# Performance work log

Hardware: AMD Instinct MI355X
Metric: run time of the kernel (lower is better)

Reference implementation:

```python
import jax, jax.numpy as jnp
import numpy as np

F_IN, H, D, C, NCLS = 1024, 512, 256, 10, 4


def setup_inputs() -> dict:
    key = jax.random.key(0)
    ks = jax.random.split(key, 20)
    N = 32768
    x_path = jax.random.normal(ks[0], (N, F_IN), dtype=jnp.float32)
    cluster_id = jax.random.randint(ks[1], (N,), 0, C, dtype=jnp.int64)
    s1 = 1.0 / np.sqrt(F_IN)
    s2 = 1.0 / np.sqrt(H)
    s3 = 1.0 / np.sqrt(D)
    return {
        "x_path": x_path,
        "cluster_id": cluster_id,
        "W1": jax.random.normal(ks[2], (C, F_IN, H), dtype=jnp.float32) * s1,
        "b1": jnp.zeros((C, H), dtype=jnp.float32),
        "W2": jax.random.normal(ks[3], (C, H, H), dtype=jnp.float32) * s2,
        "b2": jnp.zeros((C, H), dtype=jnp.float32),
        "fc_W": jax.random.normal(ks[4], (H, H), dtype=jnp.float32) * s2,
        "fc_b": jnp.zeros((H,), dtype=jnp.float32),
        "a_W": jax.random.normal(ks[5], (H, D), dtype=jnp.float32) * s2,
        "a_b": jnp.zeros((D,), dtype=jnp.float32),
        "g_W": jax.random.normal(ks[6], (H, D), dtype=jnp.float32) * s2,
        "g_b": jnp.zeros((D,), dtype=jnp.float32),
        "c_W": jax.random.normal(ks[7], (D, 1), dtype=jnp.float32) * s3,
        "c_b": jnp.zeros((1,), dtype=jnp.float32),
        "rho_W": jax.random.normal(ks[8], (H, D), dtype=jnp.float32) * s2,
        "rho_b": jnp.zeros((D,), dtype=jnp.float32),
        "cls_W": jax.random.normal(ks[9], (D, NCLS), dtype=jnp.float32) * s3,
        "cls_b": jnp.zeros((NCLS,), dtype=jnp.float32),
    }


def reference(x_path, cluster_id, W1, b1, W2, b2, fc_W, fc_b, a_W, a_b,
              g_W, g_b, c_W, c_b, rho_W, rho_b, cls_W, cls_b):
    relu = jax.nn.relu
    means = []
    for i in range(C):  # fixed small set of clusters (structurally distinct MLPs)
        m = (cluster_id == i).astype(x_path.dtype)          # [N]
        y = relu(relu(x_path @ W1[i] + b1[i]) @ W2[i] + b2[i])  # [N, H]
        cnt = jnp.maximum(m.sum(), 1.0)
        means.append((y * m[:, None]).sum(axis=0) / cnt)    # [H] segment mean
    h_cluster = jnp.stack(means, axis=0)                    # [C, H]
    h = relu(h_cluster @ fc_W + fc_b)                       # [C, H]
    a = jnp.tanh(h @ a_W + a_b)                             # [C, D]
    g = jax.nn.sigmoid(h @ g_W + g_b)                       # [C, D]
    A = (a * g) @ c_W + c_b                                 # [C, 1]
    A = jax.nn.softmax(A.T, axis=1)                         # [1, C]
    h_path = A @ h                                          # [1, H]
    h_path = relu(h_path @ rho_W + rho_b).squeeze()         # [D]
    logits = (h_path @ cls_W + cls_b)[None, :]              # [1, NCLS]
    Y_hat = jnp.argmax(logits, axis=1, keepdims=True)       # [1, 1]
    hazards = jax.nn.sigmoid(logits)
    S = jnp.cumprod(1.0 - hazards, axis=1)
    return hazards, S, Y_hat
```

## Files before the change

### kernel.cpp

```cpp
#include <hip/hip_runtime.h>
#include <hip/hip_fp16.h>
#include <math.h>

#define FIN 1024
#define H 512
#define DD 256
#define NCLS 4
#define MAXC 64

#define TMM 32
#define WCOLS 40

#define WS_TOFF 1088
#define WS_NZ   1408
#define WS_SUMS 1536

typedef _Float16 f16x8 __attribute__((ext_vector_type(8)));
typedef _Float16 f16x4 __attribute__((ext_vector_type(4)));
typedef _Float16 f16x2 __attribute__((ext_vector_type(2)));
typedef float    f32x4 __attribute__((ext_vector_type(4)));

__global__ void detect_kernel(const int* __restrict__ cid32, int* flag, int n) {
    int i = blockIdx.x * blockDim.x + threadIdx.x;
    bool p = (i < n) && (i & 1) && (cid32[i] != 0);
    unsigned long long m = __ballot(p);
    if (p && ((threadIdx.x & 63) == (__ffsll(m) - 1))) atomicOr(flag, 1);
}

__device__ __forceinline__ int get_cid(const int* cid, int flag, int i) {
    return flag ? cid[i] : cid[2 * i];
}

__global__ void count_kernel(const int* __restrict__ cid, const int* __restrict__ flag,
                             int* counts, int n, int C) {
    __shared__ int lc[MAXC];
    int tid = threadIdx.x;
    if (tid < C) lc[tid] = 0;
    __syncthreads();
    int i = blockIdx.x * blockDim.x + tid;
    if (i < n) {
        int c = get_cid(cid, *flag, i);
        if ((unsigned)c < (unsigned)C) atomicAdd(&lc[c], 1);
    }
    __syncthreads();
    if (tid < C && lc[tid] > 0) atomicAdd(&counts[tid], lc[tid]);
}

__global__ void offsets_kernel(const int* __restrict__ counts, int* offs, int* toff,
                               int C, int tilesz) {
    if (threadIdx.x == 0 && blockIdx.x == 0) {
        int s = 0, ts = 0;
        offs[0] = 0; toff[0] = 0;
        for (int c = 0; c < C; c++) {
            s += counts[c];                          offs[c + 1] = s;
            ts += (counts[c] + tilesz - 1) / tilesz; toff[c + 1] = ts;
        }
    }
}

__global__ void compact_kernel(const int* __restrict__ cid, const int* __restrict__ flag,
                               const int* __restrict__ offs, int* cursor,
                               int* lists, int n, int C) {
    __shared__ int lc[MAXC], lbase[MAXC], lpos[MAXC];
    int tid = threadIdx.x;
    if (tid < C) { lc[tid] = 0; lpos[tid] = 0; }
    __syncthreads();
    int i = blockIdx.x * blockDim.x + tid;
    int c = -1;
    if (i < n) {
        int cc = get_cid(cid, *flag, i);
        if ((unsigned)cc < (unsigned)C) { c = cc; atomicAdd(&lc[c], 1); }
    }
    __syncthreads();
    if (tid < C && lc[tid] > 0) lbase[tid] = atomicAdd(&cursor[tid], lc[tid]);
    __syncthreads();
    if (c >= 0) {
        int p = atomicAdd(&lpos[c], 1);
        lists[offs[c] + lbase[c] + p] = i;
    }
}


__device__ __forceinline__ int frag_off(int r, int g) {
    int blk = r >> 1;
    int slot = (((r & 1) << 2) | g) ^ (blk & 7);
    return blk * 128 + slot * 16;
}

__device__ __forceinline__ void gload1k(const char* g, char* l) {
    __builtin_amdgcn_global_load_lds(
        (const __attribute__((address_space(1))) void*)g,
        (__attribute__((address_space(3))) void*)l, 16, 0, 0);
}

__device__ __forceinline__ void wprep_body(
    const float* __restrict__ W, _Float16* __restrict__ hi,
    _Float16* __restrict__ lo, int K, int b, float sw[32][132], int tid)
{
    int ktn = K >> 5;
    int c = b / (4 * ktn);
    int rem = b % (4 * ktn);
    int nb = rem / ktn, kt = rem % ktn;
    const float* Wc = W + (size_t)c * K * H + (size_t)(kt * 32) * H + nb * 128;
#pragma unroll
    for (int it = 0; it < 4; it++) {
        int id = it * 256 + tid;
        int r = id >> 5, c4 = (id & 31) * 4;
        *(float4*)&sw[r][c4] = *(const float4*)(Wc + (size_t)r * H + c4);
    }
    __syncthreads();
    size_t tile = ((size_t)(c * 4 + nb)) * ktn + kt;
    char* hp = (char*)hi + tile * 8192;
    char* lp = (char*)lo + tile * 8192;
#pragma unroll
    for (int it = 0; it < 2; it++) {
        int fi = it * 256 + tid;
        int cl = fi >> 2, g = fi & 3;
        f16x8 hv, lv;
#pragma unroll
        for (int e = 0; e < 8; e++) {
            float v = sw[g * 8 + e][cl];
            _Float16 h = (_Float16)v;
            hv[e] = h;
            lv[e] = (_Float16)(v - (float)h);
        }
        int off = frag_off(cl, g);
        *(f16x8*)(hp + off) = hv;
        *(f16x8*)(lp + off) = lv;
    }
}

__global__ __launch_bounds__(256) void wprep_both(
    const float* __restrict__ W1, _Float16* __restrict__ w1h, _Float16* __restrict__ w1l,
    const float* __restrict__ W2, _Float16* __restrict__ w2h, _Float16* __restrict__ w2l,
    int C)
{
    __shared__ float sw[32][132];
    int n1 = C * 4 * (FIN / 32);
    int b = blockIdx.x;
    int tid = threadIdx.x;
    if (b < n1) wprep_body(W1, w1h, w1l, FIN, b, sw, tid);
    else        wprep_body(W2, w2h, w2l, H, b - n1, sw, tid);
}

struct __align__(16) GSmem {
    union {
        struct { _Float16 A[2][4096]; _Float16 Bh[2][4096]; _Float16 Bl[2][4096]; } s;
        _Float16 Ct[128][132];
    } u;
    int sIdx[128];
};

__global__ __launch_bounds__(256, 3) void gemm1(
    const float* __restrict__ x,
    const int* __restrict__ counts, const int* __restrict__ offs,
    const int* __restrict__ toff, const int* __restrict__ lists,
    const _Float16* __restrict__ wh, const _Float16* __restrict__ wl,
    const float* __restrict__ b1, _Float16* __restrict__ h1,
    int C, int nwg)
{
    int bid = blockIdx.x;
    {
        int q = nwg >> 3, r = nwg & 7, xcd = bid & 7, k = bid >> 3;
        bid = (xcd < r ? xcd * (q + 1) : r * (q + 1) + (xcd - r) * q) + k;
    }
    int ntile = toff[C];
    if (bid >= ntile * 4) return;
    int t = bid >> 2, nb = bid & 3;
    int c = 0;
    while (c + 1 < C && t >= toff[c + 1]) c++;
    int cnt = counts[c];
    int row0 = (t - toff[c]) * 128;

    __shared__ GSmem sm;
    int tid = threadIdx.x;
    int lane = tid & 63;
    int wave = __builtin_amdgcn_readfirstlane(tid >> 6);
    if (tid < 128) {
        int r = row0 + tid;
        sm.sIdx[tid] = (r < cnt) ? lists[offs[c] + r] : -1;
    }
    __syncthreads();

    int r0 = tid >> 2, g0 = tid & 3;
    int gi0 = sm.sIdx[r0], gi1 = sm.sIdx[64 + r0];
    const float* xp0 = x + (size_t)(gi0 < 0 ? 0 : gi0) * FIN + g0 * 8;
    const float* xp1 = x + (size_t)(gi1 < 0 ? 0 : gi1) * FIN + g0 * 8;
    int aoff0 = frag_off(r0, g0), aoff1 = frag_off(64 + r0, g0);

    const char* gh = (const char*)wh + ((size_t)(c * 4 + nb) * 32) * 8192;
    const char* gl = (const char*)wl + ((size_t)(c * 4 + nb) * 32) * 8192;
    char* ldsA  = (char*)sm.u.s.A;
    char* ldsBh = (char*)sm.u.s.Bh;
    char* ldsBl = (char*)sm.u.s.Bl;
    int ch = wave * 2;

    int wr = wave >> 1, wq = wave & 1;
    int l15 = lane & 15, g = lane >> 4;

    f32x4 acc[4][4];
#pragma unroll
    for (int i = 0; i < 4; i++)
#pragma unroll
        for (int j = 0; j < 4; j++) acc[i][j] = (f32x4){0.f, 0.f, 0.f, 0.f};

    {
        const char* gsh = gh + ch * 1024 + lane * 16;
        const char* gsl = gl + ch * 1024 + lane * 16;
        gload1k(gsh,        ldsBh + ch * 1024);
        gload1k(gsh + 1024, ldsBh + ch * 1024 + 1024);
        gload1k(gsl,        ldsBl + ch * 1024);
        gload1k(gsl + 1024, ldsBl + ch * 1024 + 1024);
        float4 v0a = make_float4(0.f,0.f,0.f,0.f), v0b = v0a, v1a = v0a, v1b = v0a;
        if (gi0 >= 0) { v0a = *(const float4*)xp0; v0b = *(const float4*)(xp0 + 4); }
        if (gi1 >= 0) { v1a = *(const float4*)xp1; v1b = *(const float4*)(xp1 + 4); }
        f16x8 a0 = { (_Float16)v0a.x, (_Float16)v0a.y, (_Float16)v0a.z, (_Float16)v0a.w,
                     (_Float16)v0b.x, (_Float16)v0b.y, (_Float16)v0b.z, (_Float16)v0b.w };
        f16x8 a1 = { (_Float16)v1a.x, (_Float16)v1a.y, (_Float16)v1a.z, (_Float16)v1a.w,
                     (_Float16)v1b.x, (_Float16)v1b.y, (_Float16)v1b.z, (_Float16)v1b.w };
        *(f16x8*)(ldsA + aoff0) = a0;
        *(f16x8*)(ldsA + aoff1) = a1;
        xp0 += 32; xp1 += 32;
    }
    __syncthreads();

    int cur = 0;
    for (int kt = 0; kt < 32; kt++) {
        int nxt = cur ^ 1;
        bool pf = kt < 31;
        float4 v0a = make_float4(0.f,0.f,0.f,0.f), v0b = v0a, v1a = v0a, v1b = v0a;
        if (pf) {
            const char* gsh = gh + (size_t)(kt + 1) * 8192 + ch * 1024 + lane * 16;
            const char* gsl = gl + (size_t)(kt + 1) * 8192 + ch * 1024 + lane * 16;
            gload1k(gsh,        ldsBh + nxt * 8192 + ch * 1024);
            gload1k(gsh + 1024, ldsBh + nxt * 8192 + ch * 1024 + 1024);
            gload1k(gsl,        ldsBl + nxt * 8192 + ch * 1024);
            gload1k(gsl + 1024, ldsBl + nxt * 8192 + ch * 1024 + 1024);
            if (gi0 >= 0) { v0a = *(const float4*)xp0; v0b = *(const float4*)(xp0 + 4); }
            if (gi1 >= 0) { v1a = *(const float4*)xp1; v1b = *(const float4*)(xp1 + 4); }
            xp0 += 32; xp1 += 32;
        }
        f16x8 a[4], bh[4], bl[4];
#pragma unroll
        for (int fr = 0; fr < 4; fr++)
            a[fr] = *(const f16x8*)(ldsA + cur * 8192 + frag_off(wr * 64 + fr * 16 + l15, g));
#pragma unroll
        for (int fc = 0; fc < 4; fc++) {
            int col = wq * 64 + fc * 16 + l15;
            bh[fc] = *(const f16x8*)(ldsBh + cur * 8192 + frag_off(col, g));
            bl[fc] = *(const f16x8*)(ldsBl + cur * 8192 + frag_off(col, g));
        }
#pragma unroll
        for (int fr = 0; fr < 4; fr++)
#pragma unroll
            for (int fc = 0; fc < 4; fc++) {
                acc[fr][fc] = __builtin_amdgcn_mfma_f32_16x16x32_f16(a[fr], bh[fc], acc[fr][fc], 0, 0, 0);
                acc[fr][fc] = __builtin_amdgcn_mfma_f32_16x16x32_f16(a[fr], bl[fc], acc[fr][fc], 0, 0, 0);
            }
        if (pf) {
            f16x8 a0 = { (_Float16)v0a.x, (_Float16)v0a.y, (_Float16)v0a.z, (_Float16)v0a.w,
                         (_Float16)v0b.x, (_Float16)v0b.y, (_Float16)v0b.z, (_Float16)v0b.w };
            f16x8 a1 = { (_Float16)v1a.x, (_Float16)v1a.y, (_Float16)v1a.z, (_Float16)v1a.w,
                         (_Float16)v1b.x, (_Float16)v1b.y, (_Float16)v1b.z, (_Float16)v1b.w };
            *(f16x8*)(ldsA + nxt * 8192 + aoff0) = a0;
            *(f16x8*)(ldsA + nxt * 8192 + aoff1) = a1;
        }
        __syncthreads();
        cur = nxt;
    }
    __syncthreads();
    const float* b1c = b1 + (size_t)c * H + nb * 128;
#pragma unroll
    for (int fc = 0; fc < 4; fc++) {
        int colL = wq * 64 + fc * 16 + l15;
        float bv = b1c[colL];
#pragma unroll
        for (int fr = 0; fr < 4; fr++)
#pragma unroll
            for (int j = 0; j < 4; j++) {
                int rowL = wr * 64 + fr * 16 + g * 4 + j;
                float v = acc[fr][fc][j] + bv;
                sm.u.Ct[rowL][colL] = (_Float16)(v > 0.f ? v : 0.f);
            }
    }
    __syncthreads();
    char* hout = (char*)h1 + ((size_t)t * 16 + nb * 4) * 8192;
#pragma unroll
    for (int ktl = 0; ktl < 4; ktl++)
#pragma unroll
        for (int it = 0; it < 2; it++) {
            int fi = it * 256 + tid;
            int rl = fi >> 2, gg = fi & 3;
            f16x8 v = *(const f16x8*)&sm.u.Ct[rl][ktl * 32 + gg * 8];
            *(f16x8*)(hout + (size_t)ktl * 8192 + frag_off(rl, gg)) = v;
        }
}

__global__ __launch_bounds__(256, 3) void gemm2(
    const _Float16* __restrict__ h1,
    const int* __restrict__ counts, const int* __restrict__ toff,
    const _Float16* __restrict__ wh, const _Float16* __restrict__ wl,
    const float* __restrict__ b2, double* __restrict__ sums,
    int C, int nwg)
{
    int bid = blockIdx.x;
    {
        int q = nwg >> 3, r = nwg & 7, xcd = bid & 7, k = bid >> 3;
        bid = (xcd < r ? xcd * (q + 1) : r * (q + 1) + (xcd - r) * q) + k;
    }
    int ntile = toff[C];
    if (bid >= ntile * 4) return;
    int t = bid >> 2, nb = bid & 3;
    int c = 0;
    while (c + 1 < C && t >= toff[c + 1]) c++;
    int cnt = counts[c];
    int row0 = (t - toff[c]) * 128;

    __shared__ alignas(16) _Float16 sA2[2][4096];
    __shared__ alignas(16) _Float16 sBh2[2][4096];
    __shared__ alignas(16) _Float16 sBl2[2][4096];

    int tid = threadIdx.x;
    int lane = tid & 63;
    int wave = __builtin_amdgcn_readfirstlane(tid >> 6);
    int wr = wave >> 1, wq = wave & 1;
    int l15 = lane & 15, g = lane >> 4;
    int ch = wave * 2;

    const char* gA = (const char*)h1 + (size_t)t * 16 * 8192;
    const char* gh = (const char*)wh + ((size_t)(c * 4 + nb) * 16) * 8192;
    const char* gl = (const char*)wl + ((size_t)(c * 4 + nb) * 16) * 8192;

    f32x4 acc[4][4];
#pragma unroll
    for (int i = 0; i < 4; i++)
#pragma unroll
        for (int j = 0; j < 4; j++) acc[i][j] = (f32x4){0.f, 0.f, 0.f, 0.f};

    {
        const char* ga  = gA + ch * 1024 + lane * 16;
        const char* gsh = gh + ch * 1024 + lane * 16;
        const char* gsl = gl + ch * 1024 + lane * 16;
        gload1k(ga,         (char*)sA2  + ch * 1024);
        gload1k(ga + 1024,  (char*)sA2  + ch * 1024 + 1024);
        gload1k(gsh,        (char*)sBh2 + ch * 1024);
        gload1k(gsh + 1024, (char*)sBh2 + ch * 1024 + 1024);
        gload1k(gsl,        (char*)sBl2 + ch * 1024);
        gload1k(gsl + 1024, (char*)sBl2 + ch * 1024 + 1024);
    }
    __syncthreads();

    int cur = 0;
    for (int kt = 0; kt < 16; kt++) {
        int nxt = cur ^ 1;
        if (kt < 15) {
            const char* ga  = gA + (size_t)(kt + 1) * 8192 + ch * 1024 + lane * 16;
            const char* gsh = gh + (size_t)(kt + 1) * 8192 + ch * 1024 + lane * 16;
            const char* gsl = gl + (size_t)(kt + 1) * 8192 + ch * 1024 + lane * 16;
            gload1k(ga,         (char*)sA2  + nxt * 8192 + ch * 1024);
            gload1k(ga + 1024,  (char*)sA2  + nxt * 8192 + ch * 1024 + 1024);
            gload1k(gsh,        (char*)sBh2 + nxt * 8192 + ch * 1024);
            gload1k(gsh + 1024, (char*)sBh2 + nxt * 8192 + ch * 1024 + 1024);
            gload1k(gsl,        (char*)sBl2 + nxt * 8192 + ch * 1024);
            gload1k(gsl + 1024, (char*)sBl2 + nxt * 8192 + ch * 1024 + 1024);
        }
        f16x8 a[4], bh[4], bl[4];
#pragma unroll
        for (int fr = 0; fr < 4; fr++)
            a[fr] = *(const f16x8*)((char*)sA2 + cur * 8192 + frag_off(wr * 64 + fr * 16 + l15, g));
#pragma unroll
        for (int fc = 0; fc < 4; fc++) {
            int col = wq * 64 + fc * 16 + l15;
            bh[fc] = *(const f16x8*)((char*)sBh2 + cur * 8192 + frag_off(col, g));
            bl[fc] = *(const f16x8*)((char*)sBl2 + cur * 8192 + frag_off(col, g));
        }
#pragma unroll
        for (int fr = 0; fr < 4; fr++)
#pragma unroll
            for (int fc = 0; fc < 4; fc++) {
                acc[fr][fc] = __builtin_amdgcn_mfma_f32_16x16x32_f16(a[fr], bh[fc], acc[fr][fc], 0, 0, 0);
                acc[fr][fc] = __builtin_amdgcn_mfma_f32_16x16x32_f16(a[fr], bl[fc], acc[fr][fc], 0, 0, 0);
            }
        __syncthreads();
        cur = nxt;
    }
    const float* b2c = b2 + (size_t)c * H + nb * 128;
    int rbound = cnt - row0;
    float psum[4];
#pragma unroll
    for (int fc = 0; fc < 4; fc++) {
        int colL = wq * 64 + fc * 16 + l15;
        float bv = b2c[colL];
        float s = 0.f;
#pragma unroll
        for (int fr = 0; fr < 4; fr++)
#pragma unroll
            for (int j = 0; j < 4; j++) {
                int rowL = wr * 64 + fr * 16 + g * 4 + j;
                float v = acc[fr][fc][j] + bv;
                v = v > 0.f ? v : 0.f;
                if (rowL < rbound) s += v;
            }
        psum[fc] = s;
    }
#pragma unroll
    for (int fc = 0; fc < 4; fc++) {
        psum[fc] += __shfl_xor(psum[fc], 16);
        psum[fc] += __shfl_xor(psum[fc], 32);
    }
    if (g == 0) {
#pragma unroll
        for (int fc = 0; fc < 4; fc++)
            atomicAdd(&sums[(size_t)c * H + nb * 128 + wq * 64 + fc * 16 + l15],
                      (double)psum[fc]);
    }
}

__global__ __launch_bounds__(256) void wsplit_kernel(
    const float* __restrict__ W, _Float16* __restrict__ hi,
    _Float16* __restrict__ lo, int K, int N)
{
    __shared__ float tile[64][65];
    int tid = threadIdx.x;
    int tilesN = N >> 6, tilesK = K >> 6;
    int b = blockIdx.x;
    int c = b / (tilesK * tilesN);
    int r = b % (tilesK * tilesN);
    int tk = r / tilesN, tn = r % tilesN;
    const float* Wc = W + (size_t)c * K * N;
    int k0 = tk << 6, n0 = tn << 6;
#pragma unroll
    for (int it = 0; it < 16; it++) {
        int id = it * 256 + tid;
        int kr = id >> 6, nc = id & 63;
        tile[kr][nc] = Wc[(size_t)(k0 + kr) * N + n0 + nc];
    }
    __syncthreads();
    _Float16* hic = hi + (size_t)c * N * K;
    _Float16* loc = lo + (size_t)c * N * K;
#pragma unroll
    for (int it = 0; it < 8; it++) {
        int id = it * 256 + tid;
        int nc = id >> 5, kp = (id & 31) * 2;
        float a0 = tile[kp][nc], a1 = tile[kp + 1][nc];
        _Float16 h0 = (_Float16)a0, h1v = (_Float16)a1;
        _Float16 l0 = (_Float16)(a0 - (float)h0);
        _Float16 l1 = (_Float16)(a1 - (float)h1v);
        size_t off = (size_t)(n0 + nc) * K + k0 + kp;
        f16x2 hv = {h0, h1v}, lv = {l0, l1};
        *(f16x2*)(hic + off) = hv;
        *(f16x2*)(loc + off) = lv;
    }
}

struct __align__(16) MfmaSmem {
    _Float16 sW[2][128][WCOLS];
    _Float16 sH[TMM][520];
    _Float16 sX[TMM][WCOLS];
    int      sIdx[TMM];
};

__global__ __launch_bounds__(256, 2) void mlp_mfma(
    const float* __restrict__ x,
    const int* __restrict__ counts, const int* __restrict__ offs,
    const int* __restrict__ toff, const int* __restrict__ lists,
    const _Float16* __restrict__ w1h, const _Float16* __restrict__ w1l,
    const _Float16* __restrict__ w2h, const _Float16* __restrict__ w2l,
    const float* __restrict__ b1, const float* __restrict__ b2,
    double* __restrict__ sums, int C, int nwg)
{
    int bid = blockIdx.x;
    {
        int q = nwg >> 3, r = nwg & 7, xcd = bid & 7, k = bid >> 3;
        bid = (xcd < r ? xcd * (q + 1) : r * (q + 1) + (xcd - r) * q) + k;
    }
    if (bid >= toff[C]) return;
    int c = 0;
    while (c + 1 < C && bid >= toff[c + 1]) c++;
    int t = bid - toff[c];
    int cnt = counts[c];
    int row0 = t * TMM;

    __shared__ MfmaSmem sm;
    int tid  = threadIdx.x;
    int lane = tid & 63, wave = tid >> 6;
    int wr = wave >> 1, wq = wave & 1;
    int l15 = lane & 15, g = lane >> 4;

    if (tid < TMM) {
        int r = row0 + tid;
        sm.sIdx[tid] = (r < cnt) ? lists[offs[c] + r] : -1;
    }

    const _Float16* w1hc = w1h + (size_t)c * FIN * H;
    const _Float16* w1lc = w1l + (size_t)c * FIN * H;
    const _Float16* w2hc = w2h + (size_t)c * H * H;
    const _Float16* w2lc = w2l + (size_t)c * H * H;
    const float* b1c = b1 + (size_t)c * H;
    const float* b2c = b2 + (size_t)c * H;

    int xr = tid >> 3;
    int xk = (tid & 7) * 4;
    int s_lc = tid >> 2;
    int s_kc = (tid & 3) * 8;

    for (int nb = 0; nb < H; nb += 128) {
        f32x4 acc[4];
#pragma unroll
        for (int f = 0; f < 4; f++) acc[f] = (f32x4){0.f, 0.f, 0.f, 0.f};

        for (int kk = 0; kk < FIN; kk += 32) {
            __syncthreads();
            {
                int gi = sm.sIdx[xr];
                float4 v = make_float4(0.f, 0.f, 0.f, 0.f);
                if (gi >= 0) v = *(const float4*)(x + (size_t)gi * FIN + kk + xk);
                f16x4 hv = { (_Float16)v.x, (_Float16)v.y, (_Float16)v.z, (_Float16)v.w };
                *(f16x4*)&sm.sX[xr][xk] = hv;
            }
            {
                const _Float16* ph = w1hc + (size_t)(nb + s_lc) * FIN + kk + s_kc;
                const _Float16* pl = w1lc + (size_t)(nb + s_lc) * FIN + kk + s_kc;
                *(f16x8*)&sm.sW[0][s_lc][s_kc]      = *(const f16x8*)ph;
                *(f16x8*)&sm.sW[0][64 + s_lc][s_kc] = *(const f16x8*)(ph + (size_t)64 * FIN);
                *(f16x8*)&sm.sW[1][s_lc][s_kc]      = *(const f16x8*)pl;
                *(f16x8*)&sm.sW[1][64 + s_lc][s_kc] = *(const f16x8*)(pl + (size_t)64 * FIN);
            }
            __syncthreads();
            f16x8 a = *(const f16x8*)&sm.sX[wr * 16 + l15][g * 8];
#pragma unroll
            for (int f = 0; f < 4; f++) {
                int lc = wq * 64 + f * 16 + l15;
                f16x8 bh = *(const f16x8*)&sm.sW[0][lc][g * 8];
                f16x8 bl = *(const f16x8*)&sm.sW[1][lc][g * 8];
                acc[f] = __builtin_amdgcn_mfma_f32_16x16x32_f16(a, bh, acc[f], 0, 0, 0);
                acc[f] = __builtin_amdgcn_mfma_f32_16x16x32_f16(a, bl, acc[f], 0, 0, 0);
            }
        }
#pragma unroll
        for (int f = 0; f < 4; f++) {
            int col = nb + wq * 64 + f * 16 + l15;
            float bv = b1c[col];
#pragma unroll
            for (int j = 0; j < 4; j++) {
                int row = wr * 16 + g * 4 + j;
                float v = acc[f][j] + bv;
                sm.sH[row][col] = (_Float16)(v > 0.f ? v : 0.f);
            }
        }
    }

    for (int nb = 0; nb < H; nb += 128) {
        f32x4 acc[4];
#pragma unroll
        for (int f = 0; f < 4; f++) acc[f] = (f32x4){0.f, 0.f, 0.f, 0.f};

        for (int kk = 0; kk < H; kk += 32) {
            __syncthreads();
            {
                const _Float16* ph = w2hc + (size_t)(nb + s_lc) * H + kk + s_kc;
                const _Float16* pl = w2lc + (size_t)(nb + s_lc) * H + kk + s_kc;
                *(f16x8*)&sm.sW[0][s_lc][s_kc]      = *(const f16x8*)ph;
                *(f16x8*)&sm.sW[0][64 + s_lc][s_kc] = *(const f16x8*)(ph + (size_t)64 * H);
                *(f16x8*)&sm.sW[1][s_lc][s_kc]      = *(const f16x8*)pl;
                *(f16x8*)&sm.sW[1][64 + s_lc][s_kc] = *(const f16x8*)(pl + (size_t)64 * H);
            }
            __syncthreads();
            f16x8 a = *(const f16x8*)&sm.sH[wr * 16 + l15][kk + g * 8];
#pragma unroll
            for (int f = 0; f < 4; f++) {
                int lc = wq * 64 + f * 16 + l15;
                f16x8 bh = *(const f16x8*)&sm.sW[0][lc][g * 8];
                f16x8 bl = *(const f16x8*)&sm.sW[1][lc][g * 8];
                acc[f] = __builtin_amdgcn_mfma_f32_16x16x32_f16(a, bh, acc[f], 0, 0, 0);
                acc[f] = __builtin_amdgcn_mfma_f32_16x16x32_f16(a, bl, acc[f], 0, 0, 0);
            }
        }
        float psum[4];
#pragma unroll
        for (int f = 0; f < 4; f++) {
            int col = nb + wq * 64 + f * 16 + l15;
            float bv = b2c[col];
            float s = 0.f;
#pragma unroll
            for (int j = 0; j < 4; j++) {
                int row = wr * 16 + g * 4 + j;
                float v = acc[f][j] + bv;
                v = v > 0.f ? v : 0.f;
                if (sm.sIdx[row] >= 0) s += v;
            }
            psum[f] = s;
        }
#pragma unroll
        for (int f = 0; f < 4; f++) {
            psum[f] += __shfl_xor(psum[f], 16);
            psum[f] += __shfl_xor(psum[f], 32);
        }
        if (g == 0) {
#pragma unroll
            for (int f = 0; f < 4; f++) {
                int col = nb + wq * 64 + f * 16 + l15;
                atomicAdd(&sums[(size_t)c * H + col], (double)psum[f]);
            }
        }
    }
}

__global__ __launch_bounds__(256) void row_mlp(
    const float* __restrict__ x, const int* __restrict__ cid,
    const int* __restrict__ flag,
    const float* __restrict__ W1, const float* __restrict__ b1,
    const float* __restrict__ W2, const float* __restrict__ b2,
    double* __restrict__ sums, int n, int C)
{
    int r = blockIdx.x;
    if (r >= n) return;
    int c = get_cid(cid, *flag, r);
    if ((unsigned)c >= (unsigned)C) return;

    __shared__ float sx[FIN];
    __shared__ float sh[H];
    int tid = threadIdx.x;

    for (int i = tid; i < FIN; i += 256) sx[i] = x[(size_t)r * FIN + i];
    __syncthreads();

    const float* W1c = W1 + (size_t)c * FIN * H;
    const float* b1c = b1 + (size_t)c * H;
    for (int col = tid; col < H; col += 256) {
        float acc = 0.f;
        for (int k = 0; k < FIN; k++) acc += sx[k] * W1c[(size_t)k * H + col];
        acc += b1c[col];
        sh[col] = acc > 0.f ? acc : 0.f;
    }
    __syncthreads();

    const float* W2c = W2 + (size_t)c * H * H;
    const float* b2c = b2 + (size_t)c * H;
    for (int col = tid; col < H; col += 256) {
        float acc = 0.f;
        for (int k = 0; k < H; k++) acc += sh[k] * W2c[(size_t)k * H + col];
        acc += b2c[col];
        float y = acc > 0.f ? acc : 0.f;
        atomicAdd(&sums[(size_t)c * H + col], (double)y);
    }
}

__global__ __launch_bounds__(128) void tailA_kernel(
    const int* __restrict__ counts, const double* __restrict__ sums,
    const float* __restrict__ fcW, const float* __restrict__ fcb,
    double* __restrict__ h_ws, int* __restrict__ nzflag)
{
    int b = blockIdx.x;
    int c = b >> 2, ch = b & 3;
    int tid = threadIdx.x;
    __shared__ double shc[H];
    double denom = fmax((double)counts[c], 1.0);
    double nz = 0.0;
    for (int i = tid; i < H; i += 128) {
        double v = sums[(size_t)c * H + i];
        nz += fabs(v);
        shc[i] = v / denom;
    }
    if (ch == 0) {
        if (__any(nz != 0.0) && (tid & 63) == 0) atomicOr(nzflag, 1);
    }
    __syncthreads();
    int col = ch * 128 + tid;
    double acc = 0.0;
#pragma unroll 16
    for (int k = 0; k < H; k++) acc += shc[k] * (double)fcW[k * H + col];
    acc += (double)fcb[col];
    h_ws[(size_t)c * H + col] = acc > 0.0 ? acc : 0.0;
}

__global__ __launch_bounds__(128) void tailB_kernel(
    const double* __restrict__ h_ws,
    const float* __restrict__ aW, const float* __restrict__ ab,
    const float* __restrict__ gW, const float* __restrict__ gb,
    double* __restrict__ ag_ws)
{
    int b = blockIdx.x;
    int c = b >> 1, dh = b & 1;
    int tid = threadIdx.x;
    __shared__ double sh[H];
    for (int i = tid; i < H; i += 128) sh[i] = h_ws[(size_t)c * H + i];
    __syncthreads();
    int d = dh * 128 + tid;
    double aa = (double)ab[d], gg = (double)gb[d];
#pragma unroll 8
    for (int k = 0; k < H; k++) {
        double hv = sh[k];
        aa += hv * (double)aW[k * DD + d];
        gg += hv * (double)gW[k * DD + d];
    }
    ag_ws[(size_t)c * DD + d] = tanh(aa) / (1.0 + exp(-gg));
}

__global__ __launch_bounds__(256) void tailC_kernel(
    const double* __restrict__ h_ws, const double* __restrict__ ag_ws,
    const float* __restrict__ cW, const float* __restrict__ cb,
    const float* __restrict__ rhoW, const float* __restrict__ rhob,
    const float* __restrict__ clsW, const float* __restrict__ clsb,
    const int* __restrict__ counts, const int* __restrict__ nzflag,
    const int* __restrict__ cid_raw, int n, int C,
    float* __restrict__ out)
{
    int tid = threadIdx.x;
    int lane = tid & 63, w = tid >> 6;
    __shared__ double sA[MAXC];
    __shared__ double shp[H];
    __shared__ double sr[DD];
    __shared__ double lgs[NCLS];

    for (int c = w; c < C; c += 4) {
        double acc = 0.0;
        for (int d = lane; d < DD; d += 64)
            acc += ag_ws[(size_t)c * DD + d] * (double)cW[d];
#pragma unroll
        for (int off = 32; off >= 1; off >>= 1) acc += __shfl_xor(acc, off);
        if (lane == 0) sA[c] = acc + (double)cb[0];
    }
    __syncthreads();
    if (tid == 0) {
        double m = sA[0];
        for (int c = 1; c < C; c++) m = fmax(m, sA[c]);
        double s = 0.0;
        for (int c = 0; c < C; c++) { sA[c] = exp(sA[c] - m); s += sA[c]; }
        for (int c = 0; c < C; c++) sA[c] /= s;
    }
    __syncthreads();
    for (int col = tid; col < H; col += 256) {
        double s = 0.0;
        for (int c = 0; c < C; c++) s += sA[c] * h_ws[(size_t)c * H + col];
        shp[col] = s;
    }
    __syncthreads();
    {
        int d = tid;
        double acc = 0.0;
#pragma unroll 16
        for (int k = 0; k < H; k++) acc += shp[k] * (double)rhoW[k * DD + d];
        acc += (double)rhob[d];
        sr[d] = acc > 0.0 ? acc : 0.0;
    }
    __syncthreads();
    for (int kk = w; kk < NCLS; kk += 4) {
        double acc = 0.0;
        for (int d = lane; d < DD; d += 64)
            acc += sr[d] * (double)clsW[d * NCLS + kk];
#pragma unroll
        for (int off = 32; off >= 1; off >>= 1) acc += __shfl_xor(acc, off);
        if (lane == 0) lgs[kk] = acc + (double)clsb[kk];
    }
    __syncthreads();
    if (tid == 0) {
        int am = 0;
        double best = lgs[0];
        double run = 1.0;
        for (int kk = 0; kk < NCLS; kk++) {
            if (lgs[kk] > best) { best = lgs[kk]; am = kk; }
            double hz = 1.0 / (1.0 + exp(-lgs[kk]));
            out[kk] = (float)hz;
            run *= (1.0 - hz);
            out[NCLS + kk] = (float)run;
        }
        long long cnt_total = 0;
        for (int c = 0; c < C; c++) cnt_total += counts[c];
        float yout;
        if (cnt_total == 0) {
            yout = 4.0e6f + (float)((cid_raw[0] & 0xFFF) + 4096 * (cid_raw[1] & 0xFFF));
        } else if (cnt_total != (long long)n) {
            yout = 2.0e6f + (float)cnt_total;
        } else if (*nzflag == 0) {
            yout = 3.0e6f;
        } else {
            yout = (float)am;
        }
        out[2 * NCLS] = yout;
    }
}

__global__ void diag_kernel(float* __restrict__ out, float code) {
    if (threadIdx.x == 0) {
        double run = 1.0;
        for (int kk = 0; kk < NCLS; kk++) {
            out[kk] = 0.5f;
            run *= 0.5;
            out[NCLS + kk] = (float)run;
        }
        out[2 * NCLS] = code;
    }
}

extern "C" void kernel_launch(void* const* d_in, const int* in_sizes, int n_in,
                              void* d_out, int out_size, void* d_ws, size_t ws_size,
                              hipStream_t stream) {
    const float* x    = (const float*)d_in[0];
    const int*   cid  = (const int*)d_in[1];
    const float* W1   = (const float*)d_in[2];
    const float* b1   = (const float*)d_in[3];
    const float* W2   = (const float*)d_in[4];
    const float* b2   = (const float*)d_in[5];
    const float* fcW  = (const float*)d_in[6];
    const float* fcb  = (const float*)d_in[7];
    const float* aW   = (const float*)d_in[8];
    const float* ab   = (const float*)d_in[9];
    const float* gW   = (const float*)d_in[10];
    const float* gb   = (const float*)d_in[11];
    const float* cW   = (const float*)d_in[12];
    const float* cb   = (const float*)d_in[13];
    const float* rhoW = (const float*)d_in[14];
    const float* rhob = (const float*)d_in[15];
    const float* clsW = (const float*)d_in[16];
    const float* clsb = (const float*)d_in[17];
    float* out = (float*)d_out;

    long long n = in_sizes[1];
    long long C = (in_sizes[7] > 0) ? (long long)in_sizes[3] / in_sizes[7] : 0;
    bool shapes_ok =
        n > 0 &&
        (long long)in_sizes[0] == n * FIN &&
        in_sizes[7] == H && in_sizes[9] == DD && in_sizes[17] == NCLS &&
        C >= 1 && C <= MAXC &&
        (long long)in_sizes[2] == C * FIN * H &&
        (long long)in_sizes[4] == C * H * H;

    size_t hws_off   = WS_SUMS + (size_t)C * H * 8;
    size_t agws_off  = hws_off + (size_t)C * H * 8;
    size_t lists_off = agws_off + (size_t)C * DD * 8;
    size_t wt_off    = (lists_off + (size_t)n * 4 + 255) & ~(size_t)255;
    size_t w1t_bytes = (size_t)C * H * FIN * 2;
    size_t w2t_bytes = (size_t)C * H * H * 2;
    size_t w1h_off   = wt_off;
    size_t w1l_off   = w1h_off + w1t_bytes;
    size_t w2h_off   = w1l_off + w1t_bytes;
    size_t w2l_off   = w2h_off + w2t_bytes;
    size_t h1_off    = (w2l_off + w2t_bytes + 255) & ~(size_t)255;
    int    nn = (int)n, CC = (int)C;
    int    ntile_ub  = (nn + 127) / 128 + CC;
    size_t h1_bytes  = (size_t)ntile_ub * 16 * 8192;
    size_t ws_full   = h1_off + h1_bytes;
    size_t ws_mid    = h1_off;
    size_t ws_row    = lists_off;

    if (!shapes_ok) {
        diag_kernel<<<1, 64, 0, stream>>>(out, 7.0e6f + (float)(C >= 0 ? C : 0));
        return;
    }
    if (ws_size < ws_row) {
        diag_kernel<<<1, 64, 0, stream>>>(
            out, 6.0e6f + (float)(ws_size > 0 ? (ws_size >> 10) : 0));
        return;
    }

    char* ws = (char*)d_ws;
    int*    counts = (int*)ws;
    int*    flag   = (int*)(ws + 256);
    int*    cursor = (int*)(ws + 512);
    int*    offs   = (int*)(ws + 768);
    int*    toff   = (int*)(ws + WS_TOFF);
    int*    nzflag = (int*)(ws + WS_NZ);
    double* sums   = (double*)(ws + WS_SUMS);
    double* h_ws   = (double*)(ws + hws_off);
    double* ag_ws  = (double*)(ws + agws_off);
    int*    lists  = (int*)(ws + lists_off);
    _Float16* w1h  = (_Float16*)(ws + w1h_off);
    _Float16* w1l  = (_Float16*)(ws + w1l_off);
    _Float16* w2h  = (_Float16*)(ws + w2h_off);
    _Float16* w2l  = (_Float16*)(ws + w2l_off);
    _Float16* h1   = (_Float16*)(ws + h1_off);

    int nb = (nn + 255) / 256;

    hipMemsetAsync(ws, 0, hws_off, stream);

    detect_kernel<<<nb, 256, 0, stream>>>(cid, flag, nn);
    count_kernel<<<nb, 256, 0, stream>>>(cid, flag, counts, nn, CC);

    if (ws_size >= ws_full) {
        offsets_kernel<<<1, 64, 0, stream>>>(counts, offs, toff, CC, 128);
        compact_kernel<<<nb, 256, 0, stream>>>(cid, flag, offs, cursor, lists, nn, CC);
        wprep_both<<<CC * 4 * (FIN / 32 + H / 32), 256, 0, stream>>>(
            W1, w1h, w1l, W2, w2h, w2l, CC);
        int grid = ntile_ub * 4;
        gemm1<<<grid, 256, 0, stream>>>(x, counts, offs, toff, lists,
                                        w1h, w1l, b1, h1, CC, grid);
        gemm2<<<grid, 256, 0, stream>>>(h1, counts, toff, w2h, w2l, b2,
                                        sums, CC, grid);
    } else if (ws_size >= ws_mid) {
        offsets_kernel<<<1, 64, 0, stream>>>(counts, offs, toff, CC, TMM);
        compact_kernel<<<nb, 256, 0, stream>>>(cid, flag, offs, cursor, lists, nn, CC);
        wsplit_kernel<<<CC * (FIN / 64) * (H / 64), 256, 0, stream>>>(W1, w1h, w1l, FIN, H);
        wsplit_kernel<<<CC * (H / 64) * (H / 64), 256, 0, stream>>>(W2, w2h, w2l, H, H);
        int nt = (nn + TMM - 1) / TMM + CC;
        mlp_mfma<<<nt, 256, 0, stream>>>(x, counts, offs, toff, lists,
                                         w1h, w1l, w2h, w2l, b1, b2,
                                         sums, CC, nt);
    } else {
        row_mlp<<<nn, 256, 0, stream>>>(x, cid, flag, W1, b1, W2, b2, sums, nn, CC);
    }

    tailA_kernel<<<CC * 4, 128, 0, stream>>>(counts, sums, fcW, fcb, h_ws, nzflag);
    tailB_kernel<<<CC * 2, 128, 0, stream>>>(h_ws, aW, ab, gW, gb, ag_ws);
    tailC_kernel<<<1, 256, 0, stream>>>(h_ws, ag_ws, cW, cb, rhoW, rhob,
                                        clsW, clsb, counts, nzflag, cid,
                                        nn, CC, out);
}
```

Baseline: 526.1 us.

## Pre-convert x to fp16 and stream gathered rows directly into LDS in gemm1

Adds a pass that converts the fp32 input x to fp16 in workspace, plus a new gemm1 that gathers the rows via global_load_lds into a swizzled LDS layout instead of loading fp32 through registers and converting. The new kernel uses a single LDS buffer so occupancy can rise to 4 blocks per SM, and it points padding rows at a zeroed row. It costs an extra full read of x and a write of a half-size copy, and it needs a larger workspace. Without that workspace it falls back to the old register-path kernel.

```diff
diff --git a/kernel.cpp b/kernel.cpp
--- a/kernel.cpp
+++ b/kernel.cpp
@@ -80,11 +80,32 @@
     }
 }
 
+__global__ __launch_bounds__(256) void xprep_kernel(
+    const float* __restrict__ x, _Float16* __restrict__ x16, long long total8)
+{
+    long long stride = (long long)gridDim.x * 256;
+    for (long long i = blockIdx.x * 256LL + threadIdx.x; i < total8; i += stride) {
+        const float* p = x + i * 8;
+        float4 a = *(const float4*)p;
+        float4 b = *(const float4*)(p + 4);
+        f16x8 v = { (_Float16)a.x, (_Float16)a.y, (_Float16)a.z, (_Float16)a.w,
+                    (_Float16)b.x, (_Float16)b.y, (_Float16)b.z, (_Float16)b.w };
+        *(f16x8*)(x16 + i * 8) = v;
+    }
+}
+
 
 __device__ __forceinline__ int frag_off(int r, int g) {
     int blk = r >> 1;
     int slot = (((r & 1) << 2) | g) ^ (blk & 7);
     return blk * 128 + slot * 16;
+}
+
+__device__ __forceinline__ void inv_frag(int idx, int& r, int& g) {
+    int blk = idx >> 3, slot = idx & 7;
+    int s = slot ^ (blk & 7);
+    r = (blk << 1) | (s >> 2);
+    g = s & 3;
 }
 
 __device__ __forceinline__ void gload1k(const char* g, char* l) {
@@ -141,6 +162,132 @@
     int tid = threadIdx.x;
     if (b < n1) wprep_body(W1, w1h, w1l, FIN, b, sw, tid);
     else        wprep_body(W2, w2h, w2l, H, b - n1, sw, tid);
+}
+
+struct __align__(16) G1Smem {
+    union {
+        struct { _Float16 A[4096]; _Float16 Bh[4096]; _Float16 Bl[4096]; } s;
+        _Float16 Ct[128][132];
+    } u;
+    int sIdx[128];
+};
+
+__global__ __launch_bounds__(256, 4) void gemm1(
+    const _Float16* __restrict__ x16, const _Float16* __restrict__ zrow,
+    const int* __restrict__ counts, const int* __restrict__ offs,
+    const int* __restrict__ toff, const int* __restrict__ lists,
+    const _Float16* __restrict__ wh, const _Float16* __restrict__ wl,
+    const float* __restrict__ b1, _Float16* __restrict__ h1,
+    int C, int nwg)
+{
+    int bid = blockIdx.x;
+    {
+        int q = nwg >> 3, r = nwg & 7, xcd = bid & 7, k = bid >> 3;
+        bid = (xcd < r ? xcd * (q + 1) : r * (q + 1) + (xcd - r) * q) + k;
+    }
+    int ntile = toff[C];
+    if (bid >= ntile * 4) return;
+    int t = bid >> 2, nb = bid & 3;
+    int c = 0;
+    while (c + 1 < C && t >= toff[c + 1]) c++;
+    int cnt = counts[c];
+    int row0 = (t - toff[c]) * 128;
+
+    __shared__ G1Smem sm;
+    int tid = threadIdx.x;
+    int lane = tid & 63;
+    int wave = __builtin_amdgcn_readfirstlane(tid >> 6);
+    if (tid < 128) {
+        int r = row0 + tid;
+        sm.sIdx[tid] = (r < cnt) ? lists[offs[c] + r] : -1;
+    }
+    __syncthreads();
+
+    int ch = wave * 2;
+    int rA0, gA0, rA1, gA1;
+    inv_frag(ch * 64 + lane, rA0, gA0);
+    inv_frag(ch * 64 + 64 + lane, rA1, gA1);
+    int gi0 = sm.sIdx[rA0], gi1 = sm.sIdx[rA1];
+    const char* srcA0 = (gi0 >= 0)
+        ? (const char*)(x16 + (size_t)gi0 * FIN) + gA0 * 16
+        : (const char*)zrow + gA0 * 16;
+    const char* srcA1 = (gi1 >= 0)
+        ? (const char*)(x16 + (size_t)gi1 * FIN) + gA1 * 16
+        : (const char*)zrow + gA1 * 16;
+
+    const char* gh = (const char*)wh + ((size_t)(c * 4 + nb) * 32) * 8192;
+    const char* gl = (const char*)wl + ((size_t)(c * 4 + nb) * 32) * 8192;
+    char* ldsA  = (char*)sm.u.s.A;
+    char* ldsBh = (char*)sm.u.s.Bh;
+    char* ldsBl = (char*)sm.u.s.Bl;
+
+    int wr = wave >> 1, wq = wave & 1;
+    int l15 = lane & 15, g = lane >> 4;
+
+    f32x4 acc[4][4];
+#pragma unroll
+    for (int i = 0; i < 4; i++)
+#pragma unroll
+        for (int j = 0; j < 4; j++) acc[i][j] = (f32x4){0.f, 0.f, 0.f, 0.f};
+
+    for (int kt = 0; kt < 32; kt++) {
+        __syncthreads();
+        {
+            gload1k(srcA0, ldsA + ch * 1024);
+            gload1k(srcA1, ldsA + ch * 1024 + 1024);
+            const char* gsh = gh + (size_t)kt * 8192 + ch * 1024 + lane * 16;
+            const char* gsl = gl + (size_t)kt * 8192 + ch * 1024 + lane * 16;
+            gload1k(gsh,        ldsBh + ch * 1024);
+            gload1k(gsh + 1024, ldsBh + ch * 1024 + 1024);
+            gload1k(gsl,        ldsBl + ch * 1024);
+            gload1k(gsl + 1024, ldsBl + ch * 1024 + 1024);
+            srcA0 += 64; srcA1 += 64;
+        }
+        __syncthreads();
+        f16x8 a[4], bh[4], bl[4];
+#pragma unroll
+        for (int fr = 0; fr < 4; fr++)
+            a[fr] = *(const f16x8*)(ldsA + frag_off(wr * 64 + fr * 16 + l15, g));
+#pragma unroll
+        for (int fc = 0; fc < 4; fc++) {
+            int col = wq * 64 + fc * 16 + l15;
+            bh[fc] = *(const f16x8*)(ldsBh + frag_off(col, g));
+            bl[fc] = *(const f16x8*)(ldsBl + frag_off(col, g));
+        }
+#pragma unroll
+        for (int fr = 0; fr < 4; fr++)
+#pragma unroll
+            for (int fc = 0; fc < 4; fc++) {
+                acc[fr][fc] = __builtin_amdgcn_mfma_f32_16x16x32_f16(a[fr], bh[fc], acc[fr][fc], 0, 0, 0);
+                acc[fr][fc] = __builtin_amdgcn_mfma_f32_16x16x32_f16(a[fr], bl[fc], acc[fr][fc], 0, 0, 0);
+            }
+    }
+    __syncthreads();
+    const float* b1c = b1 + (size_t)c * H + nb * 128;
+#pragma unroll
+    for (int fc = 0; fc < 4; fc++) {
+        int colL = wq * 64 + fc * 16 + l15;
+        float bv = b1c[colL];
+#pragma unroll
+        for (int fr = 0; fr < 4; fr++)
+#pragma unroll
+            for (int j = 0; j < 4; j++) {
+                int rowL = wr * 64 + fr * 16 + g * 4 + j;
+                float v = acc[fr][fc][j] + bv;
+                sm.u.Ct[rowL][colL] = (_Float16)(v > 0.f ? v : 0.f);
+            }
+    }
+    __syncthreads();
+    char* hout = (char*)h1 + ((size_t)t * 16 + nb * 4) * 8192;
+#pragma unroll
+    for (int ktl = 0; ktl < 4; ktl++)
+#pragma unroll
+        for (int it = 0; it < 2; it++) {
+            int fi = it * 256 + tid;
+            int rl = fi >> 2, gg = fi & 3;
+            f16x8 v = *(const f16x8*)&sm.u.Ct[rl][ktl * 32 + gg * 8];
+            *(f16x8*)(hout + (size_t)ktl * 8192 + frag_off(rl, gg)) = v;
+        }
 }
 
 struct __align__(16) GSmem {
@@ -151,7 +298,7 @@
     int sIdx[128];
 };
 
-__global__ __launch_bounds__(256, 3) void gemm1(
+__global__ __launch_bounds__(256, 3) void gemm1_reg(
     const float* __restrict__ x,
     const int* __restrict__ counts, const int* __restrict__ offs,
     const int* __restrict__ toff, const int* __restrict__ lists,
@@ -840,7 +987,11 @@
     int    nn = (int)n, CC = (int)C;
     int    ntile_ub  = (nn + 127) / 128 + CC;
     size_t h1_bytes  = (size_t)ntile_ub * 16 * 8192;
-    size_t ws_full   = h1_off + h1_bytes;
+    size_t x16_off   = (h1_off + h1_bytes + 255) & ~(size_t)255;
+    size_t x16_bytes = (size_t)n * FIN * 2;
+    size_t zrow_off  = x16_off + x16_bytes;
+    size_t ws_fullx  = zrow_off + 2048;
+    size_t ws_full   = x16_off;
     size_t ws_mid    = h1_off;
     size_t ws_row    = lists_off;
 
@@ -870,6 +1021,8 @@
     _Float16* w2h  = (_Float16*)(ws + w2h_off);
     _Float16* w2l  = (_Float16*)(ws + w2l_off);
     _Float16* h1   = (_Float16*)(ws + h1_off);
+    _Float16* x16  = (_Float16*)(ws + x16_off);
+    _Float16* zrow = (_Float16*)(ws + zrow_off);
 
     int nb = (nn + 255) / 256;
 
@@ -884,8 +1037,16 @@
         wprep_both<<<CC * 4 * (FIN / 32 + H / 32), 256, 0, stream>>>(
             W1, w1h, w1l, W2, w2h, w2l, CC);
         int grid = ntile_ub * 4;
-        gemm1<<<grid, 256, 0, stream>>>(x, counts, offs, toff, lists,
-                                        w1h, w1l, b1, h1, CC, grid);
+        if (ws_size >= ws_fullx) {
+            hipMemsetAsync(ws + zrow_off, 0, 2048, stream);
+            long long total8 = n * (FIN / 8);
+            xprep_kernel<<<2048, 256, 0, stream>>>(x, x16, total8);
+            gemm1<<<grid, 256, 0, stream>>>(x16, zrow, counts, offs, toff, lists,
+                                            w1h, w1l, b1, h1, CC, grid);
+        } else {
+            gemm1_reg<<<grid, 256, 0, stream>>>(x, counts, offs, toff, lists,
+                                                w1h, w1l, b1, h1, CC, grid);
+        }
         gemm2<<<grid, 256, 0, stream>>>(h1, counts, toff, w2h, w2l, b2,
                                         sums, CC, grid);
     } else if (ws_size >= ws_mid) {
```

After: 499.2 us. 5.1% less time.
